# Performance work log

Measured on AMD Instinct MI355X. Metric: run time of the kernel, lower is better.

The kernel has to match this reference:

```python
import jax, jax.numpy as jnp
import numpy as np

NS = 6   # stuff classes
NT = 4   # thing classes
B, N, H, W, ROI = 2, 32, 768, 768, 28
C = NS + NT
NEG = -100.0


def setup_inputs():
    key = jax.random.key(0)
    k1, k2, k3, k4, k5, k6, k7 = jax.random.split(key, 7)
    sem_logits = jax.random.normal(k1, (B, C, H, W), dtype=jnp.float32)
    roi_msk_logits = jax.random.normal(k2, (B, N, NT, ROI, ROI), dtype=jnp.float32)
    y0 = jax.random.uniform(k3, (B, N), minval=0.0, maxval=H - 240.0)
    x0 = jax.random.uniform(k4, (B, N), minval=0.0, maxval=W - 240.0)
    hb = jax.random.uniform(k5, (B, N), minval=40.0, maxval=200.0)
    wb = jax.random.uniform(k6, (B, N), minval=40.0, maxval=200.0)
    bbx = jnp.stack([y0, x0, y0 + hb, x0 + wb], axis=-1).astype(jnp.float32)
    cls = jax.random.randint(k7, (B, N), 0, NT, dtype=jnp.int32)
    return {"sem_logits": sem_logits, "roi_msk_logits": roi_msk_logits, "bbx": bbx, "cls": cls}


def _fuse_logits(sem_logits, roi_msk_logits, bbx, cls):
    """Float part of Pofusion_ONNX.forward -> po_logits [B, NS+N, H, W]."""
    Bb, Cc, Hh, Ww = sem_logits.shape
    Nn = bbx.shape[1]
    R = roi_msk_logits.shape[-1]
    yy = jnp.arange(Hh)
    xx = jnp.arange(Ww)
    # per-box mask logits of its predicted class: [B,N,R,R]
    msk = jnp.take_along_axis(roi_msk_logits, cls[:, :, None, None, None], axis=2)[:, :, 0]
    stuff = sem_logits[:, :NS]  # [B,NS,H,W]
    y0 = jnp.floor(bbx[..., 0]).astype(jnp.int32)
    x0 = jnp.floor(bbx[..., 1]).astype(jnp.int32)
    y1 = jnp.floor(bbx[..., 2]).astype(jnp.int32)
    x1 = jnp.floor(bbx[..., 3]).astype(jnp.int32)
    # ---- po_process_semantic_logits: instance canvas (uses round()+1 on max corner) ----
    y1r = (jnp.round(bbx[..., 2]) + 1.0).astype(jnp.int32)
    x1r = (jnp.round(bbx[..., 3]) + 1.0).astype(jnp.int32)
    in_y_s = (yy[None, None, :] >= y0[..., None]) & (yy[None, None, :] < y1r[..., None])  # [B,N,H]
    in_x_s = (xx[None, None, :] >= x0[..., None]) & (xx[None, None, :] < x1r[..., None])  # [B,N,W]
    thing_logit = jnp.take_along_axis(sem_logits, (cls + NS)[:, :, None, None], axis=1)   # [B,N,H,W]
    inst = jnp.where(in_y_s[:, :, :, None] & in_x_s[:, :, None, :], thing_logit, NEG)
    # ---- po_process_mask_logits: bilinear resize (align_corners=False) + paste ----
    h = jnp.maximum(y1 - y0 + 1, 1).astype(jnp.float32)
    w = jnp.maximum(x1 - x0 + 1, 1).astype(jnp.float32)
    ys = jnp.maximum(y0, 0); ye = jnp.minimum(y1 + 1, Hh)
    xs = jnp.maximum(x0, 0); xe = jnp.minimum(x1 + 1, Ww)
    in_y_m = (yy[None, None, :] >= ys[..., None]) & (yy[None, None, :] < ye[..., None])
    in_x_m = (xx[None, None, :] >= xs[..., None]) & (xx[None, None, :] < xe[..., None])
    # source coords, PyTorch half-pixel convention with lower clamp at 0
    sy = (yy[None, None, :].astype(jnp.float32) - y0[..., None] + 0.5) * (R / h[..., None]) - 0.5
    sx = (xx[None, None, :].astype(jnp.float32) - x0[..., None] + 0.5) * (R / w[..., None]) - 0.5
    sy = jnp.clip(sy, 0.0, R - 1.0)
    sx = jnp.clip(sx, 0.0, R - 1.0)
    iy0 = jnp.floor(sy).astype(jnp.int32); iy1 = jnp.minimum(iy0 + 1, R - 1); wy = sy - iy0
    ix0 = jnp.floor(sx).astype(jnp.int32); ix1 = jnp.minimum(ix0 + 1, R - 1); wx = sx - ix0
    # separable bilinear: rows first (cheap [B,N,H,R] intermediate), then columns
    m0 = jnp.take_along_axis(msk, iy0[:, :, :, None], axis=2)
    m1 = jnp.take_along_axis(msk, iy1[:, :, :, None], axis=2)
    m_y = m0 * (1.0 - wy[..., None]) + m1 * wy[..., None]          # [B,N,H,R]
    c0 = jnp.take_along_axis(m_y, ix0[:, :, None, :], axis=3)
    c1 = jnp.take_along_axis(m_y, ix1[:, :, None, :], axis=3)
    resized = c0 * (1.0 - wx[:, :, None, :]) + c1 * wx[:, :, None, :]  # [B,N,H,W]
    mask_canvas = jnp.where(in_y_m[:, :, :, None] & in_x_m[:, :, None, :], resized, NEG)
    combined = (jax.nn.sigmoid(inst) + jax.nn.sigmoid(mask_canvas)) * (inst + mask_canvas)
    return jnp.concatenate([stuff, combined], axis=1)  # [B, NS+N, H, W]


def _post(po_logits, sem_logits, cls):
    """po_assign_class_label + po_generate_seamless_output (min_stuff_area=0)."""
    b3 = jnp.arange(B)[:, None, None]
    b2 = jnp.arange(B)[:, None]
    po_pred = jnp.argmax(po_logits, axis=1)   # argmax(softmax) == argmax(logits)
    sem_pred = jnp.argmax(sem_logits, axis=1)
    thing = po_pred >= NS
    k = jnp.clip(po_pred - NS, 0, N - 1)      # instance (box) id per pixel
    # per-instance histogram of sem_pred over its region (regions are disjoint)
    hist = jnp.zeros((B, N, C), jnp.int32).at[b3, k, sem_pred].add(thing.astype(jnp.int32))
    total = hist.sum(-1)
    present = total > 0
    sem_max = jnp.argmax(hist, axis=-1).astype(jnp.int32)  # first max == torch unique order
    max_cnt = hist.max(-1)
    tmp = cls + NS
    br1 = sem_max == tmp
    br2 = (~br1) & (2 * max_cnt >= total) & (sem_max < NS) & present  # max/total >= 0.5
    sem_label = jnp.where(br2, sem_max, tmp)
    kept = present & ~br2
    idx = jnp.cumsum(present.astype(jnp.int32), axis=1) - 1  # rank among present ids
    inst_label = jnp.where(kept, idx, -1)
    po_sem = jnp.where(thing, sem_label[b3, k], po_pred.astype(jnp.int32))
    po_inst = jnp.where(thing, inst_label[b3, k], -1)
    # ---- seamless output ----
    sp = jnp.zeros((B, NS), jnp.int32).at[b3, jnp.clip(po_sem, 0, NS - 1)].add((po_sem < NS).astype(jnp.int32))
    stuff_present = sp > 0
    stuff_rank = jnp.cumsum(stuff_present.astype(jnp.int32), axis=1) - 1
    n_stuff = stuff_present.sum(1).astype(jnp.int32)  # [B]
    v = jnp.where(kept, idx, N)
    present_v = (jnp.zeros((B, N + 1), jnp.int32).at[b2, v].add(1) > 0)[:, :N]
    rank_v = jnp.cumsum(present_v.astype(jnp.int32), axis=1) - 1
    seam_inst = 1 + n_stuff[:, None, None] + rank_v[b3, jnp.clip(po_inst, 0, N - 1)]
    seam_stuff = stuff_rank[b3, jnp.clip(po_sem, 0, NS - 1)] + 1
    seam = jnp.where(po_inst >= 0, seam_inst, jnp.where(po_sem < NS, seam_stuff, 0))
    po_pred_seamless = seam.reshape(B * H, W).astype(jnp.int32)  # torch cat over batch
    # padded class list [255, sorted stuff classes..., kept instance classes...]
    L = 1 + NS + N
    po_cls = jnp.full((B, L + 1), -1, jnp.int32).at[:, 0].set(255)
    stuff_pos = jnp.where(stuff_present, 1 + stuff_rank, L)  # L = dump slot
    po_cls = po_cls.at[b2, stuff_pos].set(jnp.broadcast_to(jnp.arange(NS, dtype=jnp.int32), (B, NS)))
    rank_k = jnp.cumsum(kept.astype(jnp.int32), axis=1) - 1
    inst_pos = jnp.where(kept, 1 + n_stuff[:, None] + rank_k, L)
    po_cls = po_cls.at[b2, inst_pos].set(tmp)
    po_cls = po_cls[:, :L]
    valid_len = (1 + n_stuff + kept.sum(1)).astype(jnp.int32)
    po_iscrowd = jnp.where(jnp.arange(L)[None, :] < valid_len[:, None], 0, -1).astype(jnp.int32)
    return po_pred_seamless, po_cls, po_iscrowd, valid_len


def reference(sem_logits, roi_msk_logits, bbx, cls):
    po_logits = _fuse_logits(sem_logits, roi_msk_logits, bbx, cls)
    return _post(po_logits, sem_logits, cls)
```

## Files before the change

kernel.cpp:

```cpp
#include <hip/hip_runtime.h>
#include <math.h>

#define NSs 6
#define NTs 4
#define Bb  2
#define Nn  32
#define Hh  768
#define Ww  768
#define Rr  28
#define Cch 10
#define NCH 38
#define HW  (Hh*Ww)
#define NEGD (-100.0)
#define NKEY (Nn*Cch + NSs)

struct InstP {
  int y0, x0, y1r, x1r;
  int ys, ye, xs, xe;
  float sc_y, sc_x;
  int tc;
  int mskoff;
};

__device__ __forceinline__ double sigd(double x) { return 1.0 / (1.0 + exp(-x)); }

__device__ __forceinline__ int fuse_px(
    int y, int x, const float (&ch)[Cch], unsigned rel,
    const InstP* __restrict__ spar, const float* __restrict__ roi,
    double EPS, int* smp_out)
{
  int smp = 0; float smv = ch[0];
#pragma unroll
  for (int c = 1; c < Cch; c++) if (ch[c] > smv) { smv = ch[c]; smp = c; }
  *smp_out = smp;

  double m = (double)ch[0]; int pidx = 0;
#pragma unroll
  for (int c = 1; c < NSs; c++) { double v = (double)ch[c]; if (v > m) { m = v; pidx = c; } }

  int next_ch = NSs;
  while (rel) {
    int n = __ffs(rel) - 1; rel &= rel - 1;
    int chn_ = NSs + n;
    if (chn_ > next_ch && EPS > m) { m = EPS; pidx = next_ch; }
    next_ch = chn_ + 1;
    const InstP p = spar[n];
    bool in_i = (y >= p.y0) && (y < p.y1r) && (x >= p.x0) && (x < p.x1r);
    bool in_m = (y >= p.ys) && (y < p.ye)  && (x >= p.xs) && (x < p.xe);
    bool in_any = in_i || in_m;
    if (__any(in_any)) {
      if (in_any) {
        int tcl = p.tc;
        float tl = (tcl == 6) ? ch[6] : (tcl == 7) ? ch[7] : (tcl == 8) ? ch[8] : ch[9];
        double iv = in_i ? (double)tl : NEGD;
        double mv = NEGD;
        if (in_m) {
          double syv = ((double)(y - p.y0) + 0.5) * (double)p.sc_y - 0.5;
          double sxv = ((double)(x - p.x0) + 0.5) * (double)p.sc_x - 0.5;
          syv = fmin(fmax(syv, 0.0), 27.0);
          sxv = fmin(fmax(sxv, 0.0), 27.0);
          int iy0 = (int)syv, ix0 = (int)sxv;
          int iy1 = min(iy0 + 1, 27), ix1 = min(ix0 + 1, 27);
          double wy = syv - (double)iy0, wx = sxv - (double)ix0;
          const float* mp = roi + p.mskoff;
          double m00 = (double)mp[iy0*Rr + ix0];
          double m01 = (double)mp[iy0*Rr + ix1];
          double m10 = (double)mp[iy1*Rr + ix0];
          double m11 = (double)mp[iy1*Rr + ix1];
          double c0 = m00*(1.0 - wy) + m10*wy;
          double c1 = m01*(1.0 - wy) + m11*wy;
          mv = c0*(1.0 - wx) + c1*wx;
        }
        double s2 = iv + mv;
        if (fmax(2.0*s2, 0.0) > m) {
          double val = (sigd(iv) + sigd(mv)) * s2;
          if (val > m) { m = val; pidx = chn_; }
        }
      } else {
        if (EPS > m) { m = EPS; pidx = chn_; }
      }
    } else {
      if (EPS > m) { m = EPS; pidx = chn_; }
    }
  }
  if (next_ch < NCH && EPS > m) { m = EPS; pidx = next_ch; }
  return pidx;
}

__device__ __forceinline__ void setup_inst(
    int b, int tid, const float* __restrict__ bbx, const int* __restrict__ cls,
    InstP* spar)
{
  const int n = tid;
  const float* bbp = bbx + ((size_t)b*Nn + n)*4;
  float f0 = bbp[0], f1 = bbp[1], f2 = bbp[2], f3 = bbp[3];
  int y0 = (int)floorf(f0), x0 = (int)floorf(f1);
  int y1 = (int)floorf(f2), x1 = (int)floorf(f3);
  int y1r = (int)(rintf(f2) + 1.0f);
  int x1r = (int)(rintf(f3) + 1.0f);
  float hh = fmaxf((float)(y1 - y0 + 1), 1.0f);
  float wd = fmaxf((float)(x1 - x0 + 1), 1.0f);
  InstP p;
  p.y0 = y0; p.x0 = x0; p.y1r = y1r; p.x1r = x1r;
  p.ys = max(y0, 0); p.ye = min(y1 + 1, Hh);
  p.xs = max(x0, 0); p.xe = min(x1 + 1, Ww);
  p.sc_y = 28.0f / hh; p.sc_x = 28.0f / wd;
  int cl = cls[b*Nn + n];
  p.tc = NSs + cl;
  p.mskoff = (((b*Nn + n)*NTs) + cl)*Rr*Rr;
  spar[n] = p;
}

__global__ void k_zero(int* __restrict__ p, int n) {
  for (int i = threadIdx.x; i < n; i += 256) p[i] = 0;
}

__global__ __launch_bounds__(256) void k_fuse(
    const float* __restrict__ sem, const float* __restrict__ roi,
    const float* __restrict__ bbx, const int* __restrict__ cls,
    int* __restrict__ out_pred, int* __restrict__ g_hist, int* __restrict__ g_scount)
{
  __shared__ InstP spar[Nn];
  __shared__ int s_all[NKEY];
  __shared__ unsigned s_rel;
  __shared__ int s_xlo[Nn], s_xhi[Nn];

  const int bid  = blockIdx.x;
  const int y    = bid % Hh;
  const int b    = bid / Hh;
  const int tid  = threadIdx.x;
  const int lane = tid & 63;

  if (tid == 0) s_rel = 0u;
  for (int i = tid; i < NKEY; i += 256) s_all[i] = 0;
  if (tid < Nn) {
    setup_inst(b, tid, bbx, cls, spar);
    const InstP p = spar[tid];
    s_xlo[tid] = min(p.x0, p.xs);
    s_xhi[tid] = max(p.x1r, p.xe);
    bool rowi = (y >= p.y0) && (y < p.y1r);
    bool rowm = (y >= p.ys) && (y < p.ye);
    if (rowi || rowm) atomicOr(&s_rel, 1u << tid);
  }
  __syncthreads();

  const double EPS = (sigd(NEGD) + sigd(NEGD)) * (NEGD + NEGD);
  const float* base = sem + (size_t)b*Cch*HW + (size_t)y*Ww;

  const int  li   = lane & 31;
  const int  gxlo = s_xlo[li];
  const int  gxhi = s_xhi[li];
  const bool grow = (lane < 32) && ((s_rel >> li) & 1u);

  float cur[Cch], nxt[Cch];
#pragma unroll
  for (int c = 0; c < Cch; c++) cur[c] = base[(size_t)c*HW + tid];

  for (int ck = 0; ck < 3; ck++) {
    const int x = ck*256 + tid;
    if (ck < 2) {
#pragma unroll
      for (int c = 0; c < Cch; c++) nxt[c] = base[(size_t)c*HW + x + 256];
    }
    const int xa = x & ~63;
    unsigned relw = (unsigned)__ballot(grow && (gxlo < xa + 64) && (gxhi > xa));

    int smp;
    int pidx = fuse_px(y, x, cur, relw, spar, roi, EPS, &smp);
    out_pred[(size_t)b*HW + (size_t)y*Ww + x] = pidx;
    atomicAdd(&s_all[(pidx >= NSs) ? ((pidx - NSs)*Cch + smp) : (Nn*Cch + pidx)], 1);

    if (ck < 2) {
#pragma unroll
      for (int c = 0; c < Cch; c++) cur[c] = nxt[c];
    }
  }

  __syncthreads();
  for (int i = tid; i < NKEY; i += 256) {
    int v = s_all[i];
    if (v) {
      if (i < Nn*Cch) atomicAdd(&g_hist[b*Nn*Cch + i], v);
      else            atomicAdd(&g_scount[b*NSs + (i - Nn*Cch)], v);
    }
  }
}

__global__ __launch_bounds__(128) void k_post(
    const int* __restrict__ g_hist, const int* __restrict__ g_scount,
    const int* __restrict__ cls, int* __restrict__ lut,
    int* __restrict__ out_tail)
{
  __shared__ int sh[Bb*Nn*Cch];
  __shared__ int spc_s[Bb][NSs];
  __shared__ int pcs[Bb][40];
  const int t = threadIdx.x;
  for (int i = t; i < Bb*Nn*Cch; i += 128) sh[i] = g_hist[i];
  if (t < Bb*NSs) spc_s[t/NSs][t%NSs] = g_scount[t];
  __syncthreads();

  const int b    = t >> 6;
  const int lane = t & 63;
  const bool act = lane < Nn;

  int total = 0, mi = 0, mx = -1, tmp = 0;
  bool br2 = false, kept = false;
  if (act) {
    const int* hb = sh + b*Nn*Cch + lane*Cch;
#pragma unroll
    for (int c = 0; c < Cch; c++) { int v = hb[c]; total += v; if (v > mx) { mx = v; mi = c; } }
    tmp = cls[b*Nn + lane] + NSs;
    bool present = total > 0;
    bool b1 = (mi == tmp);
    br2  = (!b1) && (2*mx >= total) && (mi < NSs) && present;
    kept = present && !br2;
    if (br2) atomicAdd(&spc_s[b][mi], total);
  }
  __syncthreads();

  unsigned mask6 = (unsigned)(__ballot(lane < NSs && spc_s[b][lane] > 0) & 0x3Full);
  int nstuff = __popc(mask6);
  unsigned kmask = (unsigned)(__ballot(act && kept) & 0xFFFFFFFFull);
  int nk = __popc(kmask);
  int vlen = 1 + nstuff + nk;

  if (lane < NSs) lut[b*NCH + lane] = __popc(mask6 & ((1u << lane) - 1)) + 1;
  if (act) {
    int rk     = __popc(kmask & ((1u << lane) - 1));
    int srk_mi = __popc(mask6 & ((1u << mi) - 1));
    lut[b*NCH + NSs + lane] = kept ? (1 + nstuff + rk) : (br2 ? srk_mi + 1 : 0);
  }

  if (lane < 39) pcs[b][lane] = -1;
  __syncthreads();
  if (lane == 0) pcs[b][0] = 255;
  if (lane < NSs && ((mask6 >> lane) & 1))
    pcs[b][1 + __popc(mask6 & ((1u << lane) - 1))] = lane;
  if (act && kept)
    pcs[b][1 + nstuff + __popc(kmask & ((1u << lane) - 1))] = tmp;
  __syncthreads();

  int* pc = out_tail;
  int* ic = out_tail + Bb*39;
  int* vl = out_tail + 2*Bb*39;
  if (lane < 39) {
    pc[b*39 + lane] = pcs[b][lane];
    ic[b*39 + lane] = (lane < vlen) ? 0 : -1;
  }
  if (lane == 0) vl[b] = vlen;
}

__global__ __launch_bounds__(256) void k_seam(int* __restrict__ pred, const int* __restrict__ lut)
{
  __shared__ int slut[Bb*NCH];
  int tid = threadIdx.x;
  if (tid < Bb*NCH) slut[tid] = lut[tid];
  __syncthreads();
  size_t i = ((size_t)blockIdx.x*256 + tid) * 4;
  int b = (int)(i / HW);
  int4 v = *reinterpret_cast<int4*>(pred + i);
  int base = b*NCH;
  v.x = slut[base + v.x];
  v.y = slut[base + v.y];
  v.z = slut[base + v.z];
  v.w = slut[base + v.w];
  *reinterpret_cast<int4*>(pred + i) = v;
}

extern "C" void kernel_launch(void* const* d_in, const int* in_sizes, int n_in,
                              void* d_out, int out_size, void* d_ws, size_t ws_size,
                              hipStream_t stream)
{
  const float* sem = (const float*)d_in[0];
  const float* roi = (const float*)d_in[1];
  const float* bbx = (const float*)d_in[2];
  const int*   cls = (const int*)d_in[3];
  int* out = (int*)d_out;

  int* g_hist   = (int*)d_ws;
  int* g_scount = g_hist + Bb*Nn*Cch;
  int* lut      = g_scount + Bb*NSs;

  k_zero<<<1, 256, 0, stream>>>(g_hist, Bb*Nn*Cch + Bb*NSs);
  k_fuse<<<dim3(Bb*Hh), 256, 0, stream>>>(sem, roi, bbx, cls, out, g_hist, g_scount);
  k_post<<<1, 128, 0, stream>>>(g_hist, g_scount, cls, lut, out + (size_t)Bb*HW);
  k_seam<<<dim3((Bb*HW)/(256*4)), 256, 0, stream>>>(out, lut);
}
```

Baseline: 112.0 us.

## Fuse fuse/post/seam stages into one cooperative kernel with grid syncs

Replaces the four-kernel pipeline (zero, fuse, post, seam) with a single cooperative kernel of one block per image row. Each block handles both batches, keeps per-pixel argmax indices in shared memory as bytes, and remaps them through the LUT after two grid-wide syncs. This removes launch overhead and the global write plus re-read of the intermediate prediction map. In exchange it needs all 768 blocks co-resident (3 per CU), halves the number of blocks, and adds grid-sync latency. It falls back to the old path when occupancy or workspace is insufficient.

```diff
diff --git a/kernel.cpp b/kernel.cpp
--- a/kernel.cpp
+++ b/kernel.cpp
@@ -1,5 +1,8 @@
 #include <hip/hip_runtime.h>
+#include <hip/hip_cooperative_groups.h>
 #include <math.h>
+
+namespace cg = cooperative_groups;
 
 #define NSs 6
 #define NTs 4
@@ -13,6 +16,8 @@
 #define HW  (Hh*Ww)
 #define NEGD (-100.0)
 #define NKEY (Nn*Cch + NSs)
+#define WS_SC  640
+#define WS_LUT 652
 
 struct InstP {
   int y0, x0, y1r, x1r;
@@ -88,10 +93,9 @@
 }
 
 __device__ __forceinline__ void setup_inst(
-    int b, int tid, const float* __restrict__ bbx, const int* __restrict__ cls,
+    int b, int n, const float* __restrict__ bbx, const int* __restrict__ cls,
     InstP* spar)
 {
-  const int n = tid;
   const float* bbp = bbx + ((size_t)b*Nn + n)*4;
   float f0 = bbp[0], f1 = bbp[1], f2 = bbp[2], f3 = bbp[3];
   int y0 = (int)floorf(f0), x0 = (int)floorf(f1);
@@ -111,6 +115,154 @@
   spar[n] = p;
 }
 
+__global__ __launch_bounds__(256, 3) void k_all(
+    const float* __restrict__ sem, const float* __restrict__ roi,
+    const float* __restrict__ bbx, const int* __restrict__ cls,
+    int* __restrict__ out, int* __restrict__ ws)
+{
+  __shared__ InstP spar[Bb*Nn];
+  __shared__ int s_all[Bb*NKEY];
+  __shared__ unsigned s_relrow[Bb];
+  __shared__ int s_xlo[Bb*Nn], s_xhi[Bb*Nn];
+  __shared__ unsigned char s_pb[Bb*Ww];
+  __shared__ int slut2[Bb*NCH];
+  __shared__ int sh2[WS_LUT];
+  __shared__ int spc_s[Bb][NSs];
+  __shared__ int pcs[Bb][40];
+
+  cg::grid_group grid = cg::this_grid();
+
+  const int y    = blockIdx.x;
+  const int tid  = threadIdx.x;
+  const int lane = tid & 63;
+
+  if (tid < Bb) s_relrow[tid] = 0u;
+  for (int i = tid; i < Bb*NKEY; i += 256) s_all[i] = 0;
+  if (tid < Bb*Nn) {
+    const int bb = tid >> 5, n = tid & 31;
+    setup_inst(bb, n, bbx, cls, spar + bb*Nn);
+    const InstP p = spar[tid];
+    s_xlo[tid] = min(p.x0, p.xs);
+    s_xhi[tid] = max(p.x1r, p.xe);
+    bool rowi = (y >= p.y0) && (y < p.y1r);
+    bool rowm = (y >= p.ys) && (y < p.ye);
+    if (rowi || rowm) atomicOr(&s_relrow[bb], 1u << n);
+  }
+  __syncthreads();
+
+  const double EPS = (sigd(NEGD) + sigd(NEGD)) * (NEGD + NEGD);
+
+  const int  gb   = lane >> 5;
+  const int  gxlo = s_xlo[lane];
+  const int  gxhi = s_xhi[lane];
+  const bool grow = (s_relrow[gb] >> (lane & 31)) & 1u;
+
+  for (int bb = 0; bb < Bb; bb++) {
+    const float* base = sem + (size_t)bb*Cch*HW + (size_t)y*Ww;
+    const InstP* sp = spar + bb*Nn;
+    float cur[Cch], nxt[Cch];
+#pragma unroll
+    for (int c = 0; c < Cch; c++) cur[c] = base[(size_t)c*HW + tid];
+    for (int ck = 0; ck < 3; ck++) {
+      const int x = ck*256 + tid;
+      if (ck < 2) {
+#pragma unroll
+        for (int c = 0; c < Cch; c++) nxt[c] = base[(size_t)c*HW + x + 256];
+      }
+      const int xa = x & ~63;
+      unsigned long long ball = __ballot(grow && (gxlo < xa + 64) && (gxhi > xa));
+      unsigned relw = (unsigned)(ball >> (32*bb));
+
+      int smp;
+      int pidx = fuse_px(y, x, cur, relw, sp, roi, EPS, &smp);
+      s_pb[bb*Ww + x] = (unsigned char)pidx;
+      atomicAdd(&s_all[bb*NKEY + ((pidx >= NSs) ? ((pidx - NSs)*Cch + smp)
+                                                : (Nn*Cch + pidx))], 1);
+      if (ck < 2) {
+#pragma unroll
+        for (int c = 0; c < Cch; c++) cur[c] = nxt[c];
+      }
+    }
+  }
+  __syncthreads();
+  for (int i = tid; i < Bb*NKEY; i += 256) {
+    int v = s_all[i];
+    if (v) {
+      int bb = i / NKEY, k = i - bb*NKEY;
+      if (k < Nn*Cch) atomicAdd(&ws[bb*Nn*Cch + k], v);
+      else            atomicAdd(&ws[WS_SC + bb*NSs + (k - Nn*Cch)], v);
+    }
+  }
+  __threadfence();
+  grid.sync();
+
+  if (blockIdx.x == 0) {
+    for (int i = tid; i < WS_LUT; i += 256) sh2[i] = ws[i];
+    __syncthreads();
+    const int  b   = tid >> 6;
+    const int  ln  = tid & 63;
+    const int  bs  = b & 1;
+    const bool bv  = b < Bb;
+    const bool act = bv && (ln < Nn);
+    if (bv && ln < NSs) spc_s[b][ln] = sh2[WS_SC + b*NSs + ln];
+    __syncthreads();
+    int total = 0, mi = 0, mx = -1, tmp = 0;
+    bool br2 = false, kept = false;
+    if (act) {
+      const int* hb = sh2 + b*Nn*Cch + ln*Cch;
+#pragma unroll
+      for (int c = 0; c < Cch; c++) { int v = hb[c]; total += v; if (v > mx) { mx = v; mi = c; } }
+      tmp = cls[b*Nn + ln] + NSs;
+      bool present = total > 0;
+      bool b1 = (mi == tmp);
+      br2  = (!b1) && (2*mx >= total) && (mi < NSs) && present;
+      kept = present && !br2;
+      if (br2) atomicAdd(&spc_s[b][mi], total);
+    }
+    __syncthreads();
+    unsigned mask6 = (unsigned)(__ballot(bv && ln < NSs && spc_s[bs][ln] > 0) & 0x3Full);
+    int nstuff = __popc(mask6);
+    unsigned kmask = (unsigned)(__ballot(act && kept) & 0xFFFFFFFFull);
+    int nk = __popc(kmask);
+    int vlen = 1 + nstuff + nk;
+
+    if (bv && ln < NSs)
+      ws[WS_LUT + b*NCH + ln] = __popc(mask6 & ((1u << ln) - 1)) + 1;
+    if (act) {
+      int rk  = __popc(kmask & ((1u << ln) - 1));
+      int srk = __popc(mask6 & ((1u << mi) - 1));
+      ws[WS_LUT + b*NCH + NSs + ln] = kept ? (1 + nstuff + rk) : (br2 ? srk + 1 : 0);
+    }
+    if (bv && ln < 39) pcs[b][ln] = -1;
+    __syncthreads();
+    if (bv && ln == 0) pcs[b][0] = 255;
+    if (bv && ln < NSs && ((mask6 >> ln) & 1))
+      pcs[b][1 + __popc(mask6 & ((1u << ln) - 1))] = ln;
+    if (act && kept)
+      pcs[b][1 + nstuff + __popc(kmask & ((1u << ln) - 1))] = tmp;
+    __syncthreads();
+    int* pc = out + (size_t)Bb*HW;
+    int* ic = pc + Bb*39;
+    int* vl = ic + Bb*39;
+    if (bv && ln < 39) {
+      pc[b*39 + ln] = pcs[b][ln];
+      ic[b*39 + ln] = (ln < vlen) ? 0 : -1;
+    }
+    if (bv && ln == 0) vl[b] = vlen;
+  }
+  __threadfence();
+  grid.sync();
+
+  if (tid < Bb*NCH) slut2[tid] = ws[WS_LUT + tid];
+  __syncthreads();
+#pragma unroll
+  for (int bb = 0; bb < Bb; bb++)
+    for (int ck = 0; ck < 3; ck++) {
+      int x = ck*256 + tid;
+      out[(size_t)bb*HW + (size_t)y*Ww + x] = slut2[bb*NCH + s_pb[bb*Ww + x]];
+    }
+}
+
 __global__ void k_zero(int* __restrict__ p, int n) {
   for (int i = threadIdx.x; i < n; i += 256) p[i] = 0;
 }
@@ -192,11 +344,11 @@
     int* __restrict__ out_tail)
 {
   __shared__ int sh[Bb*Nn*Cch];
-  __shared__ int spc_s[Bb][NSs];
-  __shared__ int pcs[Bb][40];
+  __shared__ int spc_f[Bb][NSs];
+  __shared__ int pcf[Bb][40];
   const int t = threadIdx.x;
   for (int i = t; i < Bb*Nn*Cch; i += 128) sh[i] = g_hist[i];
-  if (t < Bb*NSs) spc_s[t/NSs][t%NSs] = g_scount[t];
+  if (t < Bb*NSs) spc_f[t/NSs][t%NSs] = g_scount[t];
   __syncthreads();
 
   const int b    = t >> 6;
@@ -214,11 +366,11 @@
     bool b1 = (mi == tmp);
     br2  = (!b1) && (2*mx >= total) && (mi < NSs) && present;
     kept = present && !br2;
-    if (br2) atomicAdd(&spc_s[b][mi], total);
-  }
-  __syncthreads();
-
-  unsigned mask6 = (unsigned)(__ballot(lane < NSs && spc_s[b][lane] > 0) & 0x3Full);
+    if (br2) atomicAdd(&spc_f[b][mi], total);
+  }
+  __syncthreads();
+
+  unsigned mask6 = (unsigned)(__ballot(lane < NSs && spc_f[b][lane] > 0) & 0x3Full);
   int nstuff = __popc(mask6);
   unsigned kmask = (unsigned)(__ballot(act && kept) & 0xFFFFFFFFull);
   int nk = __popc(kmask);
@@ -231,20 +383,20 @@
     lut[b*NCH + NSs + lane] = kept ? (1 + nstuff + rk) : (br2 ? srk_mi + 1 : 0);
   }
 
-  if (lane < 39) pcs[b][lane] = -1;
-  __syncthreads();
-  if (lane == 0) pcs[b][0] = 255;
+  if (lane < 39) pcf[b][lane] = -1;
+  __syncthreads();
+  if (lane == 0) pcf[b][0] = 255;
   if (lane < NSs && ((mask6 >> lane) & 1))
-    pcs[b][1 + __popc(mask6 & ((1u << lane) - 1))] = lane;
+    pcf[b][1 + __popc(mask6 & ((1u << lane) - 1))] = lane;
   if (act && kept)
-    pcs[b][1 + nstuff + __popc(kmask & ((1u << lane) - 1))] = tmp;
+    pcf[b][1 + nstuff + __popc(kmask & ((1u << lane) - 1))] = tmp;
   __syncthreads();
 
   int* pc = out_tail;
   int* ic = out_tail + Bb*39;
   int* vl = out_tail + 2*Bb*39;
   if (lane < 39) {
-    pc[b*39 + lane] = pcs[b][lane];
+    pc[b*39 + lane] = pcf[b][lane];
     ic[b*39 + lane] = (lane < vlen) ? 0 : -1;
   }
   if (lane == 0) vl[b] = vlen;
@@ -276,13 +428,27 @@
   const float* bbx = (const float*)d_in[2];
   const int*   cls = (const int*)d_in[3];
   int* out = (int*)d_out;
-
-  int* g_hist   = (int*)d_ws;
-  int* g_scount = g_hist + Bb*Nn*Cch;
-  int* lut      = g_scount + Bb*NSs;
-
-  k_zero<<<1, 256, 0, stream>>>(g_hist, Bb*Nn*Cch + Bb*NSs);
-  k_fuse<<<dim3(Bb*Hh), 256, 0, stream>>>(sem, roi, bbx, cls, out, g_hist, g_scount);
-  k_post<<<1, 128, 0, stream>>>(g_hist, g_scount, cls, lut, out + (size_t)Bb*HW);
-  k_seam<<<dim3((Bb*HW)/(256*4)), 256, 0, stream>>>(out, lut);
-}
+  int* wsI = (int*)d_ws;
+
+  int maxB = 0;
+  hipError_t e = hipOccupancyMaxActiveBlocksPerMultiprocessor(
+      &maxB, (const void*)k_all, 256, 0);
+  bool ok = (e == hipSuccess) && (maxB >= 3) &&
+            (ws_size >= (size_t)(WS_LUT + Bb*NCH)*4);
+  if (ok) {
+    hipMemsetAsync(wsI, 0, WS_LUT*sizeof(int), stream);
+    void* args[] = { (void*)&sem, (void*)&roi, (void*)&bbx, (void*)&cls,
+                     (void*)&out, (void*)&wsI };
+    ok = hipLaunchCooperativeKernel((const void*)k_all, dim3(Hh), dim3(256),
+                                    args, 0, stream) == hipSuccess;
+  }
+  if (!ok) {
+    int* g_hist   = wsI;
+    int* g_scount = g_hist + Bb*Nn*Cch;
+    int* lut      = g_scount + Bb*NSs;
+    k_zero<<<1, 256, 0, stream>>>(g_hist, Bb*Nn*Cch + Bb*NSs);
+    k_fuse<<<dim3(Bb*Hh), 256, 0, stream>>>(sem, roi, bbx, cls, out, g_hist, g_scount);
+    k_post<<<1, 128, 0, stream>>>(g_hist, g_scount, cls, lut, out + (size_t)Bb*HW);
+    k_seam<<<dim3((Bb*HW)/(256*4)), 256, 0, stream>>>(out, lut);
+  }
+}
```

After: 377.8 us. +237.4%, slower.

## Vectorize fuse loads per thread and merge post pass into seam kernel

Applied to the files above, without the earlier changes.

k_fuse now runs 192 threads per row, and each thread loads float4 vectors across the 10 channels to handle 4 contiguous pixels, writing one int4 result instead of three strided chunks. The relevance ballot now covers a 256-pixel span per wave. The single-block k_post kernel is removed. Every k_seam2 block now recomputes the class LUT in shared memory from the global histogram, and block 0 writes the tail outputs. This saves one launch and a global LUT round-trip, at the cost of redundant per-block setup work and coarser per-wave box culling.

```diff
diff --git a/kernel.cpp b/kernel.cpp
--- a/kernel.cpp
+++ b/kernel.cpp
@@ -88,10 +88,9 @@
 }
 
 __device__ __forceinline__ void setup_inst(
-    int b, int tid, const float* __restrict__ bbx, const int* __restrict__ cls,
+    int b, int n, const float* __restrict__ bbx, const int* __restrict__ cls,
     InstP* spar)
 {
-  const int n = tid;
   const float* bbp = bbx + ((size_t)b*Nn + n)*4;
   float f0 = bbp[0], f1 = bbp[1], f2 = bbp[2], f3 = bbp[3];
   int y0 = (int)floorf(f0), x0 = (int)floorf(f1);
@@ -115,7 +114,7 @@
   for (int i = threadIdx.x; i < n; i += 256) p[i] = 0;
 }
 
-__global__ __launch_bounds__(256) void k_fuse(
+__global__ __launch_bounds__(192) void k_fuse(
     const float* __restrict__ sem, const float* __restrict__ roi,
     const float* __restrict__ bbx, const int* __restrict__ cls,
     int* __restrict__ out_pred, int* __restrict__ g_hist, int* __restrict__ g_scount)
@@ -132,7 +131,7 @@
   const int lane = tid & 63;
 
   if (tid == 0) s_rel = 0u;
-  for (int i = tid; i < NKEY; i += 256) s_all[i] = 0;
+  for (int i = tid; i < NKEY; i += 192) s_all[i] = 0;
   if (tid < Nn) {
     setup_inst(b, tid, bbx, cls, spar);
     const InstP p = spar[tid];
@@ -147,37 +146,37 @@
   const double EPS = (sigd(NEGD) + sigd(NEGD)) * (NEGD + NEGD);
   const float* base = sem + (size_t)b*Cch*HW + (size_t)y*Ww;
 
+  float4 cur[Cch];
+#pragma unroll
+  for (int c = 0; c < Cch; c++)
+    cur[c] = *reinterpret_cast<const float4*>(base + (size_t)c*HW + 4*tid);
+
   const int  li   = lane & 31;
   const int  gxlo = s_xlo[li];
   const int  gxhi = s_xhi[li];
   const bool grow = (lane < 32) && ((s_rel >> li) & 1u);
-
-  float cur[Cch], nxt[Cch];
-#pragma unroll
-  for (int c = 0; c < Cch; c++) cur[c] = base[(size_t)c*HW + tid];
-
-  for (int ck = 0; ck < 3; ck++) {
-    const int x = ck*256 + tid;
-    if (ck < 2) {
-#pragma unroll
-      for (int c = 0; c < Cch; c++) nxt[c] = base[(size_t)c*HW + x + 256];
-    }
-    const int xa = x & ~63;
-    unsigned relw = (unsigned)__ballot(grow && (gxlo < xa + 64) && (gxhi > xa));
-
+  const int  wb   = (tid >> 6) << 8;
+  const unsigned relw =
+      (unsigned)__ballot(grow && (gxlo < wb + 256) && (gxhi > wb));
+
+  int4 vout = make_int4(0, 0, 0, 0);
+#pragma unroll
+  for (int k = 0; k < 4; k++) {
+    float ch[Cch];
+#pragma unroll
+    for (int c = 0; c < Cch; c++)
+      ch[c] = (k == 0) ? cur[c].x : (k == 1) ? cur[c].y : (k == 2) ? cur[c].z : cur[c].w;
+    const int x = 4*tid + k;
     int smp;
-    int pidx = fuse_px(y, x, cur, relw, spar, roi, EPS, &smp);
-    out_pred[(size_t)b*HW + (size_t)y*Ww + x] = pidx;
+    int pidx = fuse_px(y, x, ch, relw, spar, roi, EPS, &smp);
+    if (k == 0) vout.x = pidx; else if (k == 1) vout.y = pidx;
+    else if (k == 2) vout.z = pidx; else vout.w = pidx;
     atomicAdd(&s_all[(pidx >= NSs) ? ((pidx - NSs)*Cch + smp) : (Nn*Cch + pidx)], 1);
-
-    if (ck < 2) {
-#pragma unroll
-      for (int c = 0; c < Cch; c++) cur[c] = nxt[c];
-    }
-  }
-
-  __syncthreads();
-  for (int i = tid; i < NKEY; i += 256) {
+  }
+  *reinterpret_cast<int4*>(out_pred + (size_t)b*HW + (size_t)y*Ww + 4*tid) = vout;
+
+  __syncthreads();
+  for (int i = tid; i < NKEY; i += 192) {
     int v = s_all[i];
     if (v) {
       if (i < Nn*Cch) atomicAdd(&g_hist[b*Nn*Cch + i], v);
@@ -186,22 +185,25 @@
   }
 }
 
-__global__ __launch_bounds__(128) void k_post(
-    const int* __restrict__ g_hist, const int* __restrict__ g_scount,
-    const int* __restrict__ cls, int* __restrict__ lut,
+__global__ __launch_bounds__(256) void k_seam2(
+    int* __restrict__ pred, const int* __restrict__ g_hist,
+    const int* __restrict__ g_scount, const int* __restrict__ cls,
     int* __restrict__ out_tail)
 {
   __shared__ int sh[Bb*Nn*Cch];
-  __shared__ int spc_s[Bb][NSs];
-  __shared__ int pcs[Bb][40];
+  __shared__ int spc_f[Bb][NSs];
+  __shared__ int pcf[Bb][40];
+  __shared__ int slut[Bb*NCH];
   const int t = threadIdx.x;
-  for (int i = t; i < Bb*Nn*Cch; i += 128) sh[i] = g_hist[i];
-  if (t < Bb*NSs) spc_s[t/NSs][t%NSs] = g_scount[t];
-  __syncthreads();
-
-  const int b    = t >> 6;
-  const int lane = t & 63;
-  const bool act = lane < Nn;
+  for (int i = t; i < Bb*Nn*Cch; i += 256) sh[i] = g_hist[i];
+  if (t < Bb*NSs) spc_f[t/NSs][t%NSs] = g_scount[t];
+  __syncthreads();
+
+  const int  b    = t >> 6;
+  const int  lane = t & 63;
+  const int  bs   = b & 1;
+  const bool bv   = b < Bb;
+  const bool act  = bv && (lane < Nn);
 
   int total = 0, mi = 0, mx = -1, tmp = 0;
   bool br2 = false, kept = false;
@@ -214,56 +216,51 @@
     bool b1 = (mi == tmp);
     br2  = (!b1) && (2*mx >= total) && (mi < NSs) && present;
     kept = present && !br2;
-    if (br2) atomicAdd(&spc_s[b][mi], total);
-  }
-  __syncthreads();
-
-  unsigned mask6 = (unsigned)(__ballot(lane < NSs && spc_s[b][lane] > 0) & 0x3Full);
+    if (br2) atomicAdd(&spc_f[b][mi], total);
+  }
+  __syncthreads();
+
+  unsigned mask6 = (unsigned)(__ballot(bv && lane < NSs && spc_f[bs][lane] > 0) & 0x3Full);
   int nstuff = __popc(mask6);
   unsigned kmask = (unsigned)(__ballot(act && kept) & 0xFFFFFFFFull);
   int nk = __popc(kmask);
   int vlen = 1 + nstuff + nk;
 
-  if (lane < NSs) lut[b*NCH + lane] = __popc(mask6 & ((1u << lane) - 1)) + 1;
+  if (bv && lane < NSs)
+    slut[b*NCH + lane] = __popc(mask6 & ((1u << lane) - 1)) + 1;
   if (act) {
     int rk     = __popc(kmask & ((1u << lane) - 1));
     int srk_mi = __popc(mask6 & ((1u << mi) - 1));
-    lut[b*NCH + NSs + lane] = kept ? (1 + nstuff + rk) : (br2 ? srk_mi + 1 : 0);
-  }
-
-  if (lane < 39) pcs[b][lane] = -1;
-  __syncthreads();
-  if (lane == 0) pcs[b][0] = 255;
-  if (lane < NSs && ((mask6 >> lane) & 1))
-    pcs[b][1 + __popc(mask6 & ((1u << lane) - 1))] = lane;
+    slut[b*NCH + NSs + lane] = kept ? (1 + nstuff + rk) : (br2 ? srk_mi + 1 : 0);
+  }
+  if (bv && lane < 39) pcf[b][lane] = -1;
+  __syncthreads();
+  if (bv && lane == 0) pcf[b][0] = 255;
+  if (bv && lane < NSs && ((mask6 >> lane) & 1))
+    pcf[b][1 + __popc(mask6 & ((1u << lane) - 1))] = lane;
   if (act && kept)
-    pcs[b][1 + nstuff + __popc(kmask & ((1u << lane) - 1))] = tmp;
-  __syncthreads();
-
-  int* pc = out_tail;
-  int* ic = out_tail + Bb*39;
-  int* vl = out_tail + 2*Bb*39;
-  if (lane < 39) {
-    pc[b*39 + lane] = pcs[b][lane];
-    ic[b*39 + lane] = (lane < vlen) ? 0 : -1;
-  }
-  if (lane == 0) vl[b] = vlen;
-}
-
-__global__ __launch_bounds__(256) void k_seam(int* __restrict__ pred, const int* __restrict__ lut)
-{
-  __shared__ int slut[Bb*NCH];
-  int tid = threadIdx.x;
-  if (tid < Bb*NCH) slut[tid] = lut[tid];
-  __syncthreads();
-  size_t i = ((size_t)blockIdx.x*256 + tid) * 4;
-  int b = (int)(i / HW);
+    pcf[b][1 + nstuff + __popc(kmask & ((1u << lane) - 1))] = tmp;
+  __syncthreads();
+
+  if (blockIdx.x == 0) {
+    int* pc = out_tail;
+    int* ic = out_tail + Bb*39;
+    int* vl = out_tail + 2*Bb*39;
+    if (bv && lane < 39) {
+      pc[b*39 + lane] = pcf[b][lane];
+      ic[b*39 + lane] = (lane < vlen) ? 0 : -1;
+    }
+    if (bv && lane == 0) vl[b] = vlen;
+  }
+
+  size_t i = ((size_t)blockIdx.x*256 + t) * 4;
+  int bb = (int)(i / HW);
   int4 v = *reinterpret_cast<int4*>(pred + i);
-  int base = b*NCH;
-  v.x = slut[base + v.x];
-  v.y = slut[base + v.y];
-  v.z = slut[base + v.z];
-  v.w = slut[base + v.w];
+  int bo = bb*NCH;
+  v.x = slut[bo + v.x];
+  v.y = slut[bo + v.y];
+  v.z = slut[bo + v.z];
+  v.w = slut[bo + v.w];
   *reinterpret_cast<int4*>(pred + i) = v;
 }
 
@@ -279,10 +276,9 @@
 
   int* g_hist   = (int*)d_ws;
   int* g_scount = g_hist + Bb*Nn*Cch;
-  int* lut      = g_scount + Bb*NSs;
 
   k_zero<<<1, 256, 0, stream>>>(g_hist, Bb*Nn*Cch + Bb*NSs);
-  k_fuse<<<dim3(Bb*Hh), 256, 0, stream>>>(sem, roi, bbx, cls, out, g_hist, g_scount);
-  k_post<<<1, 128, 0, stream>>>(g_hist, g_scount, cls, lut, out + (size_t)Bb*HW);
-  k_seam<<<dim3((Bb*HW)/(256*4)), 256, 0, stream>>>(out, lut);
-}
+  k_fuse<<<dim3(Bb*Hh), 192, 0, stream>>>(sem, roi, bbx, cls, out, g_hist, g_scount);
+  k_seam2<<<dim3((Bb*HW)/(256*4)), 256, 0, stream>>>(out, g_hist, g_scount, cls,
+                                                     out + (size_t)Bb*HW);
+}
```

Result: slower. 132.6 us (+18.5%).
